# Optimization experiments

Measured on AMD Instinct MI355X. Metric: run time of the kernel, lower is better.

## Reference

```python
import jax, jax.numpy as jnp
import numpy as np


def setup_inputs() -> dict:
    key = jax.random.key(0)
    B, T, FFT, HOP = 16, 2048, 1024, 256
    n_bins = FFT // 2 + 1  # 513
    stfts = jax.random.normal(key, (B, T, n_bins, 2), dtype=jnp.float32)
    return {"stfts": stfts, "frame_length": FFT, "frame_step": HOP, "fft_length": FFT}


def reference(stfts, frame_length, frame_step, fft_length):
    # --- precomputed constants (built in the layer's build()) ---
    n = jnp.arange(fft_length, dtype=jnp.float32)
    angles = (2.0 * np.pi / fft_length) * (n[:, None] * n[None, :])  # [fft, fft]
    idft_cos = jnp.cos(angles)
    idft_sin = jnp.sin(angles)
    # periodic Hann window
    t = jnp.arange(frame_length, dtype=jnp.float32)
    window = 0.5 - 0.5 * jnp.cos(2.0 * np.pi * t / frame_length)
    hop_ratio = frame_step / frame_length
    normalization = np.sqrt(1.0 / (1.0 - hop_ratio + 1e-8))
    syn_window = window / np.float32(normalization)
    if fft_length > frame_length:
        syn_window = jnp.pad(syn_window, (0, fft_length - frame_length))

    # --- forward ---
    real_part = stfts[..., 0]  # [B, T, n_bins]
    imag_part = stfts[..., 1]
    if fft_length % 2 == 0:
        mirror_real = real_part[:, :, 1:-1]
        mirror_imag = imag_part[:, :, 1:-1]
    else:
        mirror_real = real_part[:, :, 1:]
        mirror_imag = imag_part[:, :, 1:]
    full_real = jnp.concatenate([real_part, mirror_real[:, :, ::-1]], axis=-1)   # [B, T, fft]
    full_imag = jnp.concatenate([imag_part, -mirror_imag[:, :, ::-1]], axis=-1)  # [B, T, fft]

    # explicit IDFT via dense matmul (transpose_b in TF; matrices are symmetric)
    time_real = jnp.einsum('btf,nf->btn', full_real, idft_cos)
    time_real = time_real - jnp.einsum('btf,nf->btn', full_imag, idft_sin)
    time_real = time_real / jnp.float32(fft_length)

    windowed = (time_real * syn_window[None, None, :])[:, :, :frame_length]  # [B, T, frame_length]

    # overlap-and-add
    B, T, L = windowed.shape
    out_len = (T - 1) * frame_step + frame_length
    idx = jnp.arange(T)[:, None] * frame_step + jnp.arange(L)[None, :]  # [T, L]
    out = jnp.zeros((B, out_len), dtype=windowed.dtype).at[:, idx].add(windowed)
    return out
```

## Files before the change

### kernel.cpp

```cpp
#include <hip/hip_runtime.h>
#include <math.h>


#define BATCH  16
#define TFR    2048
#define NB     513
#define HOP    256
#define OUTLEN 525056
#define TROWS  2051
#define OWN    32
#define NBLK   65
#define OLALEN (OWN * HOP)
#define OLAPAD (OLALEN + OLALEN / 16)

#define NTHR   512
#define NWAVE  8

#define PIDX(n) ((n) + ((n) >> 4))

#define TWO_PI 6.2831853071795864f
#define WSCALE 8.456302966727588e-4f

__device__ __forceinline__ float2 cadd(float2 a, float2 b){ return make_float2(a.x+b.x, a.y+b.y); }
__device__ __forceinline__ float2 csub(float2 a, float2 b){ return make_float2(a.x-b.x, a.y-b.y); }
__device__ __forceinline__ float2 cmul(float2 a, float2 b){ return make_float2(a.x*b.x - a.y*b.y, a.x*b.y + a.y*b.x); }

#if __has_builtin(__builtin_amdgcn_permlane32_swap)
#define HAVE_PL32 1
__device__ __forceinline__ float plsel32(float v, bool pick0) {
    auto r = __builtin_amdgcn_permlane32_swap(
        __builtin_bit_cast(int, v), __builtin_bit_cast(int, v), false, false);
    return __builtin_bit_cast(float, pick0 ? r[0] : r[1]);
}
#else
#define HAVE_PL32 0
#endif

#if __has_builtin(__builtin_amdgcn_permlane16_swap)
#define HAVE_PL16 1
__device__ __forceinline__ float plsel16(float v, bool pick0) {
    auto r = __builtin_amdgcn_permlane16_swap(
        __builtin_bit_cast(int, v), __builtin_bit_cast(int, v), false, false);
    return __builtin_bit_cast(float, pick0 ? r[0] : r[1]);
}
#else
#define HAVE_PL16 0
#endif

template<int CTRL>
__device__ __forceinline__ float dppf(float v) {
    return __builtin_bit_cast(float,
        __builtin_amdgcn_update_dpp(0, __builtin_bit_cast(int, v), CTRL, 0xF, 0xF, true));
}
__device__ __forceinline__ float swz4(float v) {
    return __builtin_bit_cast(float,
        __builtin_amdgcn_ds_swizzle(__builtin_bit_cast(int, v), 0x101F));
}

__device__ __forceinline__ float2 bstep(float2 u, float2 p, bool hi, float2 W) {
    const float2 s = cadd(u, p);
    const float2 d = cmul(csub(u, p), W);
    return hi ? d : s;
}

__device__ __constant__ const float W16C[8] = { 1.f, 0.9238795325112867f, 0.7071067811865476f, 0.3826834323650898f,
                                                0.f,-0.3826834323650898f,-0.7071067811865476f,-0.9238795325112867f };
__device__ __constant__ const float W16S[8] = { 0.f, 0.3826834323650898f, 0.7071067811865476f, 0.9238795325112867f,
                                                1.f, 0.9238795325112867f, 0.7071067811865476f, 0.3826834323650898f };
__device__ __constant__ const float CWT[16] = {
    1.f, 0.9999811752826011f, 0.9999247018391445f, 0.9998305817958234f,
    0.9996988186962042f, 0.9995294175010931f, 0.9993223845883495f, 0.9990777277526454f,
    0.9987954562051724f, 0.9984755805732948f, 0.9981181129001492f, 0.9977230666441916f,
    0.9972904566786902f, 0.9968202992911657f, 0.9963126121827780f, 0.9957674144676598f };
__device__ __constant__ const float SWT[16] = {
    0.f, 0.0061358846491545f, 0.0122715382857199f, 0.0184067299058048f,
    0.0245412285229123f, 0.0306748031766366f, 0.0368072229413588f, 0.0429382569349408f,
    0.0490676743274180f, 0.0551952443496899f, 0.0613207363022086f, 0.0674439195636641f,
    0.0735645635996674f, 0.0796824379714301f, 0.0857973123444399f, 0.0919089564971327f };

__global__ __launch_bounds__(NTHR)
void istft_rfft(const float2* __restrict__ stfts, float* __restrict__ out)
{
    __shared__ float ola[OLAPAD];

    const int tid  = threadIdx.x;
    const int lane = tid & 63;
    const int wave = tid >> 6;

    const int b  = blockIdx.x / NBLK;
    const int ib = blockIdx.x - b * NBLK;
    const int T0 = ib * OWN;

    for (int i = tid; i < OLAPAD; i += NTHR) ola[i] = 0.f;

    float2 P, V;
    { float s, c; sincosf(TWO_PI * (float)lane * (1.0f/1024.0f), &s, &c); P = make_float2(c, s); }
    const int brl = ((lane & 1) << 5) | ((lane & 2) << 3) | ((lane & 4) << 1)
                  | ((lane & 8) >> 1) | ((lane & 16) >> 3) | ((lane & 32) >> 5);
    const int n0 = brl * 16;
    { float s, c; sincosf(TWO_PI * (float)n0 * (1.0f/1024.0f), &s, &c); V = make_float2(c, s); }

    const float2 Q   = cmul(P, P);
    const float2 P4  = cmul(Q, Q);
    const float2 P8  = cmul(P4, P4);
    const float2 B64 = cmul(P8, P8);
    const float2 B32 = cmul(B64, B64);
    const float2 B16 = cmul(B32, B32);
    const float2 B8c = cmul(B16, B16);
    const float2 B4c = cmul(B8c, B8c);

#if HAVE_PL32
    bool pick32;
    { auto pr = __builtin_amdgcn_permlane32_swap(lane, lane, false, false);
      pick32 = (pr[0] == (lane ^ 32)); }
#endif
#if HAVE_PL16
    bool pick16;
    { auto pr = __builtin_amdgcn_permlane16_swap(lane, lane, false, false);
      pick16 = (pr[0] == (lane ^ 16)); }
#endif
    const bool hi32 = lane >= 32;
    const bool hi16 = (lane & 16) != 0;
    const bool hi8  = (lane & 8)  != 0;
    const bool hi4  = (lane & 4)  != 0;
    const bool hi2  = (lane & 2)  != 0;
    const bool hi1  = (lane & 1)  != 0;

    __syncthreads();

    const int tmin = (T0 - 3 > 0) ? T0 - 3 : 0;
    const int tmax = (T0 + OWN - 1 < TFR - 1) ? T0 + OWN - 1 : TFR - 1;

    auto frameProc = [&](const float2* X, const float2* XM, int t) {
        float2 Z[8];
        #pragma unroll
        for (int r = 0; r < 8; ++r) {
            const float2 mv = XM[r];
            float Yy = X[r].y, Cy = -mv.y;
            if (lane == 0 && r == 0) { Yy = 0.f; Cy = 0.f; }
            const float Sx = X[r].x + mv.x, Sy = Yy + Cy;
            const float Dx = X[r].x - mv.x, Dy = Yy - Cy;
            const float2 W = cmul(P, make_float2(W16C[r], W16S[r]));
            const float ex = W.x * Dx - W.y * Dy;
            const float ey = W.x * Dy + W.y * Dx;
            Z[r] = make_float2(Sx - ey, Sy + ex);
        }

        float2 u[8];
        {
            const float2 t0 = cadd(Z[0], Z[4]), t1 = csub(Z[0], Z[4]);
            const float2 t2 = cadd(Z[2], Z[6]), t3 = csub(Z[2], Z[6]);
            const float2 t4 = cadd(Z[1], Z[5]), t5 = csub(Z[1], Z[5]);
            const float2 t6 = cadd(Z[3], Z[7]), t7 = csub(Z[3], Z[7]);
            const float2 E0 = cadd(t0, t2), E2 = csub(t0, t2);
            const float2 E1 = make_float2(t1.x - t3.y, t1.y + t3.x);
            const float2 E3 = make_float2(t1.x + t3.y, t1.y - t3.x);
            const float2 O0 = cadd(t4, t6), O2 = csub(t4, t6);
            const float2 O1 = make_float2(t5.x - t7.y, t5.y + t7.x);
            const float2 O3 = make_float2(t5.x + t7.y, t5.y - t7.x);
            const float cc = 0.70710678118654752f;
            const float2 W1O1 = make_float2(cc * (O1.x - O1.y), cc * (O1.x + O1.y));
            const float2 iO2  = make_float2(-O2.y, O2.x);
            const float2 W3O3 = make_float2(cc * (-O3.x - O3.y), cc * (O3.x - O3.y));
            u[0] = cadd(E0, O0);   u[4] = csub(E0, O0);
            u[1] = cadd(E1, W1O1); u[5] = csub(E1, W1O1);
            u[2] = cadd(E2, iO2);  u[6] = csub(E2, iO2);
            u[3] = cadd(E3, W3O3); u[7] = csub(E3, W3O3);
        }
        {
            const float2 om3 = cmul(P4, Q);
            const float2 om5 = cmul(P8, Q);
            const float2 om6 = cmul(P8, P4);
            const float2 om7 = cmul(P8, om3);
            u[1] = cmul(u[1], Q);
            u[2] = cmul(u[2], P4);
            u[3] = cmul(u[3], om3);
            u[4] = cmul(u[4], P8);
            u[5] = cmul(u[5], om5);
            u[6] = cmul(u[6], om6);
            u[7] = cmul(u[7], om7);
        }

        #pragma unroll
        for (int m = 0; m < 8; ++m) {
            float2 p;
#if HAVE_PL32
            p = make_float2(plsel32(u[m].x, pick32), plsel32(u[m].y, pick32));
#else
            p = make_float2(__shfl_xor(u[m].x, 32), __shfl_xor(u[m].y, 32));
#endif
            u[m] = bstep(u[m], p, hi32, B64);
        }
        #pragma unroll
        for (int m = 0; m < 8; ++m) {
            float2 p;
#if HAVE_PL16
            p = make_float2(plsel16(u[m].x, pick16), plsel16(u[m].y, pick16));
#else
            p = make_float2(__shfl_xor(u[m].x, 16), __shfl_xor(u[m].y, 16));
#endif
            u[m] = bstep(u[m], p, hi16, B32);
        }
        #pragma unroll
        for (int m = 0; m < 8; ++m) {
            const float2 p = make_float2(dppf<0x128>(u[m].x), dppf<0x128>(u[m].y));
            u[m] = bstep(u[m], p, hi8, B16);
        }
        #pragma unroll
        for (int m = 0; m < 8; ++m) {
            const float2 p = make_float2(swz4(u[m].x), swz4(u[m].y));
            u[m] = bstep(u[m], p, hi4, B8c);
        }
        #pragma unroll
        for (int m = 0; m < 8; ++m) {
            const float2 p = make_float2(dppf<0x4E>(u[m].x), dppf<0x4E>(u[m].y));
            u[m] = bstep(u[m], p, hi2, B4c);
        }
        #pragma unroll
        for (int m = 0; m < 8; ++m) {
            const float2 p = make_float2(dppf<0xB1>(u[m].x), dppf<0xB1>(u[m].y));
            u[m] = hi1 ? csub(p, u[m]) : cadd(u[m], p);
        }

        const int base = (t - T0) * HOP + n0;
        if ((unsigned)base < OLALEN) {
            const int pb = PIDX(base);
            #pragma unroll
            for (int m = 0; m < 8; ++m) {
                const float w0 = 0.5f * WSCALE * (1.f - (V.x * CWT[2*m]   - V.y * SWT[2*m]));
                const float w1 = 0.5f * WSCALE * (1.f - (V.x * CWT[2*m+1] - V.y * SWT[2*m+1]));
                atomicAdd(&ola[pb + 2*m],     u[m].x * w0);
                atomicAdd(&ola[pb + 2*m + 1], u[m].y * w1);
            }
        }
    };

    for (int t = tmin + wave; t <= tmax; t += 2 * NWAVE) {
        const int  tb = t + NWAVE;
        const bool vb = (tb <= tmax);

        const float2* Ga = stfts + (size_t)(b * TFR + t) * NB;
        const float2* Gb = stfts + (size_t)(b * TFR + (vb ? tb : t)) * NB;

        float2 Xa[8], Ma[8], Xb[8], Mb[8];
        #pragma unroll
        for (int r = 0; r < 8; ++r) {
            Xa[r] = Ga[lane + 64 * r];
            Ma[r] = Ga[512 - 64 * r - lane];
        }
        #pragma unroll
        for (int r = 0; r < 8; ++r) {
            Xb[r] = Gb[lane + 64 * r];
            Mb[r] = Gb[512 - 64 * r - lane];
        }

        frameProc(Xa, Ma, t);
        if (vb) frameProc(Xb, Mb, tb);
    }

    __syncthreads();

    const int ownRows = (TROWS - T0 < OWN) ? (TROWS - T0) : OWN;
    const int total   = ownRows * HOP;
    float* og = out + (size_t)b * OUTLEN + (size_t)T0 * HOP;
    for (int i = tid; i < total; i += NTHR)
        og[i] = ola[PIDX(i)];
}

extern "C" void kernel_launch(void* const* d_in, const int* in_sizes, int n_in,
                              void* d_out, int out_size, void* d_ws, size_t ws_size,
                              hipStream_t stream)
{
    const float2* stfts = reinterpret_cast<const float2*>(d_in[0]);
    float* out = reinterpret_cast<float*>(d_out);

    istft_rfft<<<dim3(BATCH * NBLK), dim3(NTHR), 0, stream>>>(stfts, out);
}
```

Measured before the change: 203.9 us.

## Pack two real frames into one complex 1024-point FFT per wave

```diff
diff --git a/kernel.cpp b/kernel.cpp
--- a/kernel.cpp
+++ b/kernel.cpp
@@ -24,6 +24,8 @@
 __device__ __forceinline__ float2 cadd(float2 a, float2 b){ return make_float2(a.x+b.x, a.y+b.y); }
 __device__ __forceinline__ float2 csub(float2 a, float2 b){ return make_float2(a.x-b.x, a.y-b.y); }
 __device__ __forceinline__ float2 cmul(float2 a, float2 b){ return make_float2(a.x*b.x - a.y*b.y, a.x*b.y + a.y*b.x); }
+__device__ __forceinline__ float2 cmuli(float2 a){ return make_float2(-a.y, a.x); }
+__device__ __forceinline__ float2 cmulni(float2 a){ return make_float2(a.y, -a.x); }
 
 #if __has_builtin(__builtin_amdgcn_permlane32_swap)
 #define HAVE_PL32 1
@@ -63,10 +65,6 @@
     return hi ? d : s;
 }
 
-__device__ __constant__ const float W16C[8] = { 1.f, 0.9238795325112867f, 0.7071067811865476f, 0.3826834323650898f,
-                                                0.f,-0.3826834323650898f,-0.7071067811865476f,-0.9238795325112867f };
-__device__ __constant__ const float W16S[8] = { 0.f, 0.3826834323650898f, 0.7071067811865476f, 0.9238795325112867f,
-                                                1.f, 0.9238795325112867f, 0.7071067811865476f, 0.3826834323650898f };
 __device__ __constant__ const float CWT[16] = {
     1.f, 0.9999811752826011f, 0.9999247018391445f, 0.9998305817958234f,
     0.9996988186962042f, 0.9995294175010931f, 0.9993223845883495f, 0.9990777277526454f,
@@ -78,8 +76,11 @@
     0.0490676743274180f, 0.0551952443496899f, 0.0613207363022086f, 0.0674439195636641f,
     0.0735645635996674f, 0.0796824379714301f, 0.0857973123444399f, 0.0919089564971327f };
 
+#define SL0 0
+#define SLS {0,4,8,12,1,5,9,13,2,6,10,14,3,7,11,15}
+
 __global__ __launch_bounds__(NTHR)
-void istft_rfft(const float2* __restrict__ stfts, float* __restrict__ out)
+void istft_rfft2(const float2* __restrict__ stfts, float* __restrict__ out)
 {
     __shared__ float ola[OLAPAD];
 
@@ -100,10 +101,10 @@
     const int n0 = brl * 16;
     { float s, c; sincosf(TWO_PI * (float)n0 * (1.0f/1024.0f), &s, &c); V = make_float2(c, s); }
 
-    const float2 Q   = cmul(P, P);
-    const float2 P4  = cmul(Q, Q);
-    const float2 P8  = cmul(P4, P4);
-    const float2 B64 = cmul(P8, P8);
+    const float2 Qt  = cmul(P, P);
+    const float2 P4t = cmul(Qt, Qt);
+    const float2 P8t = cmul(P4t, P4t);
+    const float2 B64 = cmul(P8t, P8t);
     const float2 B32 = cmul(B64, B64);
     const float2 B16 = cmul(B32, B32);
     const float2 B8c = cmul(B16, B16);
@@ -128,134 +129,134 @@
 
     __syncthreads();
 
-    const int tmin = (T0 - 3 > 0) ? T0 - 3 : 0;
-    const int tmax = (T0 + OWN - 1 < TFR - 1) ? T0 + OWN - 1 : TFR - 1;
-
-    auto frameProc = [&](const float2* X, const float2* XM, int t) {
-        float2 Z[8];
+    const int tmin   = (T0 - 3 > 0) ? T0 - 3 : 0;
+    const int tmax   = (T0 + OWN - 1 < TFR - 1) ? T0 + OWN - 1 : TFR - 1;
+    const int npairs = (tmax - tmin + 2) >> 1;
+
+    static constexpr int SL[16] = SLS;
+
+    for (int pi = wave; pi < npairs; pi += NWAVE) {
+        const int  ta = tmin + 2 * pi;
+        const int  tb = ta + 1;
+        const bool vb = (tb <= tmax);
+
+        const float2* Ga = stfts + (size_t)(b * TFR + ta) * NB;
+        const float2* Gb = stfts + (size_t)(b * TFR + (vb ? tb : ta)) * NB;
+
+        float2 Aa[8], Ab[8], Da[8], Db[8];
+        #pragma unroll
+        for (int r = 0; r < 8; ++r) { Aa[r] = Ga[lane + 64 * r];       Ab[r] = Gb[lane + 64 * r]; }
+        #pragma unroll
+        for (int r = 0; r < 8; ++r) { Da[r] = Ga[512 - 64 * r - lane]; Db[r] = Gb[512 - 64 * r - lane]; }
+
+        float2 z[16];
+        #pragma unroll
+        for (int q = 0; q < 8; ++q) {
+            float ya = Aa[q].y, yb = Ab[q].y;
+            if (lane == 0 && q == 0) { ya = 0.f; yb = 0.f; }
+            z[q] = make_float2(Aa[q].x - yb, ya + Ab[q].x);
+        }
         #pragma unroll
         for (int r = 0; r < 8; ++r) {
-            const float2 mv = XM[r];
-            float Yy = X[r].y, Cy = -mv.y;
-            if (lane == 0 && r == 0) { Yy = 0.f; Cy = 0.f; }
-            const float Sx = X[r].x + mv.x, Sy = Yy + Cy;
-            const float Dx = X[r].x - mv.x, Dy = Yy - Cy;
-            const float2 W = cmul(P, make_float2(W16C[r], W16S[r]));
-            const float ex = W.x * Dx - W.y * Dy;
-            const float ey = W.x * Dy + W.y * Dx;
-            Z[r] = make_float2(Sx - ey, Sy + ex);
-        }
-
-        float2 u[8];
+            float may = Da[r].y, mby = Db[r].y;
+            if (lane == 0 && r == 0) { may = 0.f; mby = 0.f; }
+            z[8 + r] = make_float2(Da[r].x + mby, Db[r].x - may);
+        }
+
+        #pragma unroll
+        for (int q0 = 0; q0 < 4; ++q0) {
+            const float2 a = z[q0], bb = z[q0+4], c = z[q0+8], d = z[q0+12];
+            const float2 s0 = cadd(a, c), d0 = csub(a, c);
+            const float2 s1 = cadd(bb, d), d1 = csub(bb, d);
+            z[q0]      = cadd(s0, s1);
+            z[q0 + 4]  = cadd(d0, cmuli(d1));
+            z[q0 + 8]  = csub(s0, s1);
+            z[q0 + 12] = cadd(d0, cmulni(d1));
+        }
         {
-            const float2 t0 = cadd(Z[0], Z[4]), t1 = csub(Z[0], Z[4]);
-            const float2 t2 = cadd(Z[2], Z[6]), t3 = csub(Z[2], Z[6]);
-            const float2 t4 = cadd(Z[1], Z[5]), t5 = csub(Z[1], Z[5]);
-            const float2 t6 = cadd(Z[3], Z[7]), t7 = csub(Z[3], Z[7]);
-            const float2 E0 = cadd(t0, t2), E2 = csub(t0, t2);
-            const float2 E1 = make_float2(t1.x - t3.y, t1.y + t3.x);
-            const float2 E3 = make_float2(t1.x + t3.y, t1.y - t3.x);
-            const float2 O0 = cadd(t4, t6), O2 = csub(t4, t6);
-            const float2 O1 = make_float2(t5.x - t7.y, t5.y + t7.x);
-            const float2 O3 = make_float2(t5.x + t7.y, t5.y - t7.x);
-            const float cc = 0.70710678118654752f;
-            const float2 W1O1 = make_float2(cc * (O1.x - O1.y), cc * (O1.x + O1.y));
-            const float2 iO2  = make_float2(-O2.y, O2.x);
-            const float2 W3O3 = make_float2(cc * (-O3.x - O3.y), cc * (O3.x - O3.y));
-            u[0] = cadd(E0, O0);   u[4] = csub(E0, O0);
-            u[1] = cadd(E1, W1O1); u[5] = csub(E1, W1O1);
-            u[2] = cadd(E2, iO2);  u[6] = csub(E2, iO2);
-            u[3] = cadd(E3, W3O3); u[7] = csub(E3, W3O3);
+            const float2 W1 = make_float2(0.9238795325112867f, 0.3826834323650898f);
+            const float2 W2 = make_float2(0.7071067811865476f, 0.7071067811865476f);
+            const float2 W3 = make_float2(0.3826834323650898f, 0.9238795325112867f);
+            const float2 W6 = make_float2(-0.7071067811865476f, 0.7071067811865476f);
+            const float2 W9 = make_float2(-0.9238795325112867f, -0.3826834323650898f);
+            z[5]  = cmul(z[5],  W1);  z[6]  = cmul(z[6],  W2);  z[7]  = cmul(z[7],  W3);
+            z[9]  = cmul(z[9],  W2);  z[10] = cmuli(z[10]);     z[11] = cmul(z[11], W6);
+            z[13] = cmul(z[13], W3);  z[14] = cmul(z[14], W6);  z[15] = cmul(z[15], W9);
+        }
+        #pragma unroll
+        for (int m0 = 0; m0 < 4; ++m0) {
+            const float2 a = z[4*m0], bb = z[4*m0+1], c = z[4*m0+2], d = z[4*m0+3];
+            const float2 s0 = cadd(a, c), d0 = csub(a, c);
+            const float2 s1 = cadd(bb, d), d1 = csub(bb, d);
+            z[4*m0]     = cadd(s0, s1);
+            z[4*m0 + 1] = cadd(d0, cmuli(d1));
+            z[4*m0 + 2] = csub(s0, s1);
+            z[4*m0 + 3] = cadd(d0, cmulni(d1));
         }
         {
-            const float2 om3 = cmul(P4, Q);
-            const float2 om5 = cmul(P8, Q);
-            const float2 om6 = cmul(P8, P4);
-            const float2 om7 = cmul(P8, om3);
-            u[1] = cmul(u[1], Q);
-            u[2] = cmul(u[2], P4);
-            u[3] = cmul(u[3], om3);
-            u[4] = cmul(u[4], P8);
-            u[5] = cmul(u[5], om5);
-            u[6] = cmul(u[6], om6);
-            u[7] = cmul(u[7], om7);
-        }
-
-        #pragma unroll
-        for (int m = 0; m < 8; ++m) {
+            float2 tw = P;
+            z[SL[1]] = cmul(z[SL[1]], tw);
+            #pragma unroll
+            for (int m = 2; m < 16; ++m) {
+                tw = cmul(tw, P);
+                z[SL[m]] = cmul(z[SL[m]], tw);
+            }
+        }
+
+        #pragma unroll
+        for (int m = 0; m < 16; ++m) {
             float2 p;
 #if HAVE_PL32
-            p = make_float2(plsel32(u[m].x, pick32), plsel32(u[m].y, pick32));
-#else
-            p = make_float2(__shfl_xor(u[m].x, 32), __shfl_xor(u[m].y, 32));
-#endif
-            u[m] = bstep(u[m], p, hi32, B64);
-        }
-        #pragma unroll
-        for (int m = 0; m < 8; ++m) {
+            p = make_float2(plsel32(z[m].x, pick32), plsel32(z[m].y, pick32));
+#else
+            p = make_float2(__shfl_xor(z[m].x, 32), __shfl_xor(z[m].y, 32));
+#endif
+            z[m] = bstep(z[m], p, hi32, B64);
+        }
+        #pragma unroll
+        for (int m = 0; m < 16; ++m) {
             float2 p;
 #if HAVE_PL16
-            p = make_float2(plsel16(u[m].x, pick16), plsel16(u[m].y, pick16));
-#else
-            p = make_float2(__shfl_xor(u[m].x, 16), __shfl_xor(u[m].y, 16));
-#endif
-            u[m] = bstep(u[m], p, hi16, B32);
-        }
-        #pragma unroll
-        for (int m = 0; m < 8; ++m) {
-            const float2 p = make_float2(dppf<0x128>(u[m].x), dppf<0x128>(u[m].y));
-            u[m] = bstep(u[m], p, hi8, B16);
-        }
-        #pragma unroll
-        for (int m = 0; m < 8; ++m) {
-            const float2 p = make_float2(swz4(u[m].x), swz4(u[m].y));
-            u[m] = bstep(u[m], p, hi4, B8c);
-        }
-        #pragma unroll
-        for (int m = 0; m < 8; ++m) {
-            const float2 p = make_float2(dppf<0x4E>(u[m].x), dppf<0x4E>(u[m].y));
-            u[m] = bstep(u[m], p, hi2, B4c);
-        }
-        #pragma unroll
-        for (int m = 0; m < 8; ++m) {
-            const float2 p = make_float2(dppf<0xB1>(u[m].x), dppf<0xB1>(u[m].y));
-            u[m] = hi1 ? csub(p, u[m]) : cadd(u[m], p);
-        }
-
-        const int base = (t - T0) * HOP + n0;
-        if ((unsigned)base < OLALEN) {
-            const int pb = PIDX(base);
-            #pragma unroll
-            for (int m = 0; m < 8; ++m) {
-                const float w0 = 0.5f * WSCALE * (1.f - (V.x * CWT[2*m]   - V.y * SWT[2*m]));
-                const float w1 = 0.5f * WSCALE * (1.f - (V.x * CWT[2*m+1] - V.y * SWT[2*m+1]));
-                atomicAdd(&ola[pb + 2*m],     u[m].x * w0);
-                atomicAdd(&ola[pb + 2*m + 1], u[m].y * w1);
-            }
-        }
-    };
-
-    for (int t = tmin + wave; t <= tmax; t += 2 * NWAVE) {
-        const int  tb = t + NWAVE;
-        const bool vb = (tb <= tmax);
-
-        const float2* Ga = stfts + (size_t)(b * TFR + t) * NB;
-        const float2* Gb = stfts + (size_t)(b * TFR + (vb ? tb : t)) * NB;
-
-        float2 Xa[8], Ma[8], Xb[8], Mb[8];
-        #pragma unroll
-        for (int r = 0; r < 8; ++r) {
-            Xa[r] = Ga[lane + 64 * r];
-            Ma[r] = Ga[512 - 64 * r - lane];
-        }
-        #pragma unroll
-        for (int r = 0; r < 8; ++r) {
-            Xb[r] = Gb[lane + 64 * r];
-            Mb[r] = Gb[512 - 64 * r - lane];
-        }
-
-        frameProc(Xa, Ma, t);
-        if (vb) frameProc(Xb, Mb, tb);
+            p = make_float2(plsel16(z[m].x, pick16), plsel16(z[m].y, pick16));
+#else
+            p = make_float2(__shfl_xor(z[m].x, 16), __shfl_xor(z[m].y, 16));
+#endif
+            z[m] = bstep(z[m], p, hi16, B32);
+        }
+        #pragma unroll
+        for (int m = 0; m < 16; ++m) {
+            const float2 p = make_float2(dppf<0x128>(z[m].x), dppf<0x128>(z[m].y));
+            z[m] = bstep(z[m], p, hi8, B16);
+        }
+        #pragma unroll
+        for (int m = 0; m < 16; ++m) {
+            const float2 p = make_float2(swz4(z[m].x), swz4(z[m].y));
+            z[m] = bstep(z[m], p, hi4, B8c);
+        }
+        #pragma unroll
+        for (int m = 0; m < 16; ++m) {
+            const float2 p = make_float2(dppf<0x4E>(z[m].x), dppf<0x4E>(z[m].y));
+            z[m] = bstep(z[m], p, hi2, B4c);
+        }
+        #pragma unroll
+        for (int m = 0; m < 16; ++m) {
+            const float2 p = make_float2(dppf<0xB1>(z[m].x), dppf<0xB1>(z[m].y));
+            z[m] = hi1 ? csub(p, z[m]) : cadd(z[m], p);
+        }
+
+        const int  base_a = (ta - T0) * HOP + n0;
+        const int  base_b = base_a + HOP;
+        const bool da = (unsigned)base_a < OLALEN;
+        const bool db = vb && ((unsigned)base_b < OLALEN);
+        const int  pa = PIDX(base_a);
+        const int  pb = PIDX(base_b);
+        #pragma unroll
+        for (int m = 0; m < 16; ++m) {
+            const float2 uz = z[SL[m]];
+            const float  w  = 0.5f * WSCALE * (1.f - (V.x * CWT[m] - V.y * SWT[m]));
+            if (da) atomicAdd(&ola[pa + m], uz.x * w);
+            if (db) atomicAdd(&ola[pb + m], uz.y * w);
+        }
     }
 
     __syncthreads();
@@ -274,5 +275,5 @@
     const float2* stfts = reinterpret_cast<const float2*>(d_in[0]);
     float* out = reinterpret_cast<float*>(d_out);
 
-    istft_rfft<<<dim3(BATCH * NBLK), dim3(NTHR), 0, stream>>>(stfts, out);
-}
+    istft_rfft2<<<dim3(BATCH * NBLK), dim3(NTHR), 0, stream>>>(stfts, out);
+}
```

After: 220.5 us. 1.08x slower.
